# Performance work log

Measured on AMD Instinct MI355X. Metric: run time of the kernel, lower is better.

Reference implementation:

```python
import jax, jax.numpy as jnp
import numpy as np
import math

B, T, C, H = 4, 2048, 768, 12
D = C // H  # 64 head dim

def setup_inputs() -> dict:
    key = jax.random.key(0)
    k1, k2, k3 = jax.random.split(key, 3)
    x = jax.random.normal(k1, (B, T, C), dtype=jnp.float32)
    mask = jnp.tril(jnp.ones((T, T), dtype=bool))[None, None, :, :]  # causal [1,1,T,T]
    W_attn = jax.random.normal(k2, (C, 3 * C), dtype=jnp.float32) * 0.02
    b_attn = jnp.zeros((3 * C,), dtype=jnp.float32)
    W_proj = jax.random.normal(k3, (C, C), dtype=jnp.float32) * (0.02 / math.sqrt(2 * 12))
    b_proj = jnp.zeros((C,), dtype=jnp.float32)
    return {"x": x, "mask": mask, "W_attn": W_attn, "b_attn": b_attn,
            "W_proj": W_proj, "b_proj": b_proj}

def reference(x, mask, W_attn, b_attn, W_proj, b_proj):
    Bx, Tx, Cx = x.shape
    qkv = x @ W_attn + b_attn                       # [B,T,3C]
    qkv = qkv.reshape(Bx, Tx, 3 * H, D).transpose(0, 2, 1, 3)  # [B,3H,T,D]
    q, k, v = jnp.array_split(qkv, 3, axis=1)       # each [B,H,T,D]
    att = jnp.einsum('bhqd,bhkd->bhqk', q, k) / math.sqrt(D)  # [B,H,T,T]
    att = jnp.where(mask == 0, -jnp.inf, att)
    att = jax.nn.softmax(att, axis=-1)
    y = jnp.einsum('bhqk,bhkd->bhqd', att, v)       # [B,H,T,D]
    y = y.transpose(0, 2, 1, 3).reshape(Bx, Tx, Cx)
    return y @ W_proj + b_proj
```

## Files before the change

### kernel.cpp

```cpp
#include <hip/hip_runtime.h>
#include <math.h>

#define BB 4
#define TT 2048
#define CC 768
#define HH 12
#define DD 64
#define RS (3 * CC)

typedef __bf16 bf16x8 __attribute__((ext_vector_type(8)));
typedef float f32x4 __attribute__((ext_vector_type(4)));
typedef unsigned short u16x8 __attribute__((ext_vector_type(8)));

union U8 { bf16x8 v; u16x8 s; unsigned short u[8]; };
union BCV { __bf16 h; unsigned short u; };

__device__ __forceinline__ unsigned short f2bf(float f) {
  union { float f; unsigned u; } x; x.f = f;
  unsigned r = x.u + 0x7fffu + ((x.u >> 16) & 1u);
  return (unsigned short)(r >> 16);
}

#define AS1 __attribute__((address_space(1)))
#define AS3 __attribute__((address_space(3)))
__device__ __forceinline__ void gl_lds16(const void* g, void* l) {
  __builtin_amdgcn_global_load_lds((const AS1 unsigned int*)g,
                                   (AS3 unsigned int*)l, 16, 0, 0);
}

__global__ __launch_bounds__(256) void cvt_bf16_kernel(
    const float* __restrict__ in, unsigned short* __restrict__ out, int n8) {
  int i = blockIdx.x * 256 + threadIdx.x;
  const int stride = gridDim.x * 256;
  for (; i < n8; i += stride) {
    const float4 a = reinterpret_cast<const float4*>(in)[i * 2];
    const float4 b = reinterpret_cast<const float4*>(in)[i * 2 + 1];
    U8 p;
    p.u[0] = f2bf(a.x); p.u[1] = f2bf(a.y); p.u[2] = f2bf(a.z); p.u[3] = f2bf(a.w);
    p.u[4] = f2bf(b.x); p.u[5] = f2bf(b.y); p.u[6] = f2bf(b.z); p.u[7] = f2bf(b.w);
    reinterpret_cast<u16x8*>(out)[i] = p.s;
  }
}

__global__ __launch_bounds__(256) void transpose_cvt_kernel(
    const float* __restrict__ in, unsigned short* __restrict__ out,
    int K, int N) {
  __shared__ float T[64][65];
  const int k0 = blockIdx.y * 64, n0 = blockIdx.x * 64;
  const int tid = threadIdx.x;
  const int ty = tid >> 4, tx4 = (tid & 15) * 4;
#pragma unroll
  for (int i = 0; i < 4; ++i) {
    const int r = ty + i * 16;
    const float4 v = *reinterpret_cast<const float4*>(
        &in[(size_t)(k0 + r) * N + n0 + tx4]);
    T[r][tx4] = v.x; T[r][tx4 + 1] = v.y; T[r][tx4 + 2] = v.z; T[r][tx4 + 3] = v.w;
  }
  __syncthreads();
  const int nrow = tid >> 2, kc = (tid & 3) * 16;
  U8 p0, p1;
#pragma unroll
  for (int i = 0; i < 8; ++i) {
    p0.u[i] = f2bf(T[kc + i][nrow]);
    p1.u[i] = f2bf(T[kc + 8 + i][nrow]);
  }
  unsigned short* o = &out[(size_t)(n0 + nrow) * K + k0 + kc];
  *reinterpret_cast<u16x8*>(o) = p0.s;
  *reinterpret_cast<u16x8*>(o + 8) = p1.s;
}

__global__ __launch_bounds__(256) void vtrans_kernel(
    const unsigned short* __restrict__ qkvb, unsigned short* __restrict__ Vg) {
  __shared__ unsigned short Tt[64][72];
  const int tok0 = blockIdx.x * 64;
  const int bh = blockIdx.y, b = bh / HH, h = bh % HH;
  const int tid = threadIdx.x;
  const int r = tid >> 2, c = (tid & 3) * 16;
  const unsigned short* src =
      qkvb + (size_t)(b * TT + tok0 + r) * RS + (2 * HH + h) * DD + c;
  *reinterpret_cast<u16x8*>(&Tt[r][c]) = *reinterpret_cast<const u16x8*>(src);
  *reinterpret_cast<u16x8*>(&Tt[r][c + 8]) =
      *reinterpret_cast<const u16x8*>(src + 8);
  __syncthreads();
  const int d = tid >> 2, tc = (tid & 3) * 16;
  U8 o0, o1;
#pragma unroll
  for (int i = 0; i < 8; ++i) {
    o0.u[i] = Tt[tc + i][d];
    o1.u[i] = Tt[tc + 8 + i][d];
  }
  unsigned short* dst = Vg + ((size_t)bh * DD + d) * TT + tok0 + tc;
  *reinterpret_cast<u16x8*>(dst) = o0.s;
  *reinterpret_cast<u16x8*>(dst + 8) = o1.s;
}

template <typename OutT>
__global__ __launch_bounds__(256) void gemm_mfma_kernel(
    const unsigned short* __restrict__ A, const unsigned short* __restrict__ Bt,
    const float* __restrict__ bias, OutT* __restrict__ C,
    int M, int N, int K) {
  __shared__ unsigned short As[2][128 * 32];
  __shared__ unsigned short Bs[2][128 * 32];

  const int tid = threadIdx.x;
  const int w = tid >> 6, l = tid & 63, lr = l & 15, lg = l >> 4;
  const int wr = w >> 1, wc = w & 1;
  const int brow = blockIdx.y * 128, bcol = blockIdx.x * 128;

  f32x4 acc[4][4];
#pragma unroll
  for (int i = 0; i < 4; ++i)
#pragma unroll
    for (int j = 0; j < 4; ++j) acc[i][j] = (f32x4)(0.f);

  const int r0 = tid >> 2, c8 = (tid & 3) * 8;
  const unsigned short* gA = A + (size_t)(brow + r0) * K + c8;
  const unsigned short* gB = Bt + (size_t)(bcol + r0) * K + c8;

  gl_lds16(gA, As[0] + w * 512);
  gl_lds16(gA + (size_t)64 * K, As[0] + w * 512 + 2048);
  gl_lds16(gB, Bs[0] + w * 512);
  gl_lds16(gB + (size_t)64 * K, Bs[0] + w * 512 + 2048);
  __syncthreads();

  int cur = 0;
  for (int k0 = 0; k0 < K; k0 += 32) {
    if (k0 + 32 < K) {
      const int kn = k0 + 32;
      gl_lds16(gA + kn, As[cur ^ 1] + w * 512);
      gl_lds16(gA + (size_t)64 * K + kn, As[cur ^ 1] + w * 512 + 2048);
      gl_lds16(gB + kn, Bs[cur ^ 1] + w * 512);
      gl_lds16(gB + (size_t)64 * K + kn, Bs[cur ^ 1] + w * 512 + 2048);
    }

    bf16x8 af[4], bf[4];
#pragma unroll
    for (int mf = 0; mf < 4; ++mf)
      af[mf] = *reinterpret_cast<const bf16x8*>(
          &As[cur][(wr * 64 + mf * 16 + lr) * 32 + lg * 8]);
#pragma unroll
    for (int nf = 0; nf < 4; ++nf)
      bf[nf] = *reinterpret_cast<const bf16x8*>(
          &Bs[cur][(wc * 64 + nf * 16 + lr) * 32 + lg * 8]);
#pragma unroll
    for (int mf = 0; mf < 4; ++mf)
#pragma unroll
      for (int nf = 0; nf < 4; ++nf)
        acc[mf][nf] = __builtin_amdgcn_mfma_f32_16x16x32_bf16(
            af[mf], bf[nf], acc[mf][nf], 0, 0, 0);

    __syncthreads();
    cur ^= 1;
  }

#pragma unroll
  for (int nf = 0; nf < 4; ++nf) {
    const int col = bcol + wc * 64 + nf * 16 + lr;
    const float bv = bias[col];
#pragma unroll
    for (int mf = 0; mf < 4; ++mf) {
      const int row0 = brow + wr * 64 + mf * 16 + lg * 4;
#pragma unroll
      for (int r = 0; r < 4; ++r) {
        const float v = acc[mf][nf][r] + bv;
        if constexpr (sizeof(OutT) == 2)
          C[(size_t)(row0 + r) * N + col] = (OutT)f2bf(v);
        else
          C[(size_t)(row0 + r) * N + col] = (OutT)v;
      }
    }
  }
}

constexpr int KVT = 64;

__global__ __launch_bounds__(256) void attn_mfma_kernel(
    const unsigned short* __restrict__ qkv,
    const unsigned short* __restrict__ Vg,
    unsigned short* __restrict__ y) {
  __shared__ unsigned short Ks[KVT * 64];
  __shared__ unsigned short Vt[DD * 64];
  __shared__ unsigned short Pl[4 * 16 * 64];

  const int tid = threadIdx.x;
  const int w = tid >> 6, l = tid & 63;
  const int lr = l & 15, lg = l >> 4;
  const int bh = blockIdx.x, b = bh / HH, h = bh % HH;
  const int g = 31 - blockIdx.y;
  const int qw = g * 64 + w * 16;

  const unsigned short* qbase = qkv + (size_t)b * TT * RS + h * DD;
  const unsigned short* kbase = qkv + (size_t)b * TT * RS + (HH + h) * DD;
  const unsigned short* vgb = Vg + (size_t)bh * DD * TT;

  const float qscale = 0.125f * 1.44269504f;
  const int e = lg ^ (lr & 7);
  const int e4 = e ^ 4;

  bf16x8 qf[2];
  {
    const unsigned short* qrow = qbase + (size_t)(qw + lr) * RS;
    qf[0] = *reinterpret_cast<const bf16x8*>(qrow + lg * 8);
    qf[1] = *reinterpret_cast<const bf16x8*>(qrow + lg * 8 + 32);
  }

  f32x4 O[4];
  f32x4 ls = (f32x4)(0.f);
#pragma unroll
  for (int nb = 0; nb < 4; ++nb) O[nb] = (f32x4)(0.f);

  const int srow = tid >> 2, sc2 = (tid & 3) * 2;
  const int sw = srow & 7;
  const int sidx0 = srow * 64 + 8 * (sc2 ^ sw);
  const int sidx1 = srow * 64 + 8 * ((sc2 + 1) ^ sw);
  const int scol = (tid & 3) * 16;
  const unsigned short* kptr = kbase + (size_t)srow * RS + scol;
  const unsigned short* vptr = vgb + (size_t)srow * TT + scol;

  const int ntiles = g + 1;
  u16x8 kr0 = *reinterpret_cast<const u16x8*>(kptr);
  u16x8 kr1 = *reinterpret_cast<const u16x8*>(kptr + 8);
  u16x8 vr0 = *reinterpret_cast<const u16x8*>(vptr);
  u16x8 vr1 = *reinterpret_cast<const u16x8*>(vptr + 8);

  for (int t = 0; t < ntiles; ++t) {
    const int kv0 = t * KVT;
    __syncthreads();
    *reinterpret_cast<u16x8*>(&Ks[sidx0]) = kr0;
    *reinterpret_cast<u16x8*>(&Ks[sidx1]) = kr1;
    *reinterpret_cast<u16x8*>(&Vt[sidx0]) = vr0;
    *reinterpret_cast<u16x8*>(&Vt[sidx1]) = vr1;
    if (t + 1 < ntiles) {
      kptr += (size_t)KVT * RS;
      vptr += KVT;
      kr0 = *reinterpret_cast<const u16x8*>(kptr);
      kr1 = *reinterpret_cast<const u16x8*>(kptr + 8);
      vr0 = *reinterpret_cast<const u16x8*>(vptr);
      vr1 = *reinterpret_cast<const u16x8*>(vptr + 8);
    }
    __syncthreads();

    const bool diag = (t == g);
    const int nbmax = diag ? (w + 1) : 4;

    f32x4 s[4];
#pragma unroll
    for (int nb = 0; nb < 4; ++nb) s[nb] = (f32x4)(0.f);
    __builtin_amdgcn_s_setprio(1);
#pragma unroll
    for (int nb = 0; nb < 4; ++nb) {
      if (nb >= nbmax) continue;
      const int krow = (nb * 16 + lr) * 64;
      const bf16x8 k0 = *reinterpret_cast<const bf16x8*>(&Ks[krow + 8 * e]);
      const bf16x8 k1 = *reinterpret_cast<const bf16x8*>(&Ks[krow + 8 * e4]);
      s[nb] = __builtin_amdgcn_mfma_f32_16x16x32_bf16(qf[0], k0, s[nb], 0, 0, 0);
      s[nb] = __builtin_amdgcn_mfma_f32_16x16x32_bf16(qf[1], k1, s[nb], 0, 0, 0);
    }
    __builtin_amdgcn_s_setprio(0);

    if (diag) {
      const int qrow = qw + lg * 4;
#pragma unroll
      for (int nb = 0; nb < 4; ++nb) {
        if (nb >= nbmax) continue;
        const int key = kv0 + nb * 16 + lr;
#pragma unroll
        for (int r = 0; r < 4; ++r)
          if (key > qrow + r) s[nb][r] = -1e30f;
      }
    }
#pragma unroll
    for (int r = 0; r < 4; ++r) {
      const int prow = lg * 4 + r;
      const int pswz = (prow & 7) << 3;
      unsigned short* pbase = &Pl[w * 1024 + prow * 64];
#pragma unroll
      for (int nb = 0; nb < 4; ++nb) {
        if (nb >= nbmax) {
          pbase[(nb * 16 + lr) ^ pswz] = 0;
          continue;
        }
        const float p = exp2f(s[nb][r] * qscale);
        ls[r] += p;
        BCV cv; cv.h = (__bf16)p;
        pbase[(nb * 16 + lr) ^ pswz] = cv.u;
      }
    }

    asm volatile("s_waitcnt lgkmcnt(0)" ::: "memory");

    {
      const unsigned short* pw = &Pl[w * 1024];
      const bf16x8 pa0 = *reinterpret_cast<const bf16x8*>(&pw[lr * 64 + 8 * e]);
      const bf16x8 pa1 = *reinterpret_cast<const bf16x8*>(&pw[lr * 64 + 8 * e4]);
      __builtin_amdgcn_s_setprio(1);
#pragma unroll
      for (int nb = 0; nb < 4; ++nb) {
        const int vrow = (nb * 16 + lr) * 64;
        const bf16x8 v0 = *reinterpret_cast<const bf16x8*>(&Vt[vrow + 8 * e]);
        const bf16x8 v1 = *reinterpret_cast<const bf16x8*>(&Vt[vrow + 8 * e4]);
        O[nb] = __builtin_amdgcn_mfma_f32_16x16x32_bf16(pa0, v0, O[nb], 0, 0, 0);
        O[nb] = __builtin_amdgcn_mfma_f32_16x16x32_bf16(pa1, v1, O[nb], 0, 0, 0);
      }
      __builtin_amdgcn_s_setprio(0);
    }
  }

#pragma unroll
  for (int off = 1; off < 16; off <<= 1)
#pragma unroll
    for (int r = 0; r < 4; ++r) ls[r] += __shfl_xor(ls[r], off, 64);
  f32x4 inv;
#pragma unroll
  for (int r = 0; r < 4; ++r) inv[r] = 1.f / ls[r];
#pragma unroll
  for (int nb = 0; nb < 4; ++nb)
#pragma unroll
    for (int r = 0; r < 4; ++r)
      y[((size_t)b * TT + qw + lg * 4 + r) * CC + h * DD + nb * 16 + lr] =
          f2bf(O[nb][r] * inv[r]);
}

extern "C" void kernel_launch(void* const* d_in, const int* in_sizes, int n_in,
                              void* d_out, int out_size, void* d_ws, size_t ws_size,
                              hipStream_t stream) {
  const float* x      = (const float*)d_in[0];
  const float* W_attn = (const float*)d_in[2];
  const float* b_attn = (const float*)d_in[3];
  const float* W_proj = (const float*)d_in[4];
  const float* b_proj = (const float*)d_in[5];
  float* out = (float*)d_out;

  const int M = BB * TT;
  unsigned short* qkvb = (unsigned short*)d_ws;
  unsigned short* xb   = qkvb + (size_t)M * RS;
  unsigned short* yb   = xb + (size_t)M * CC;
  unsigned short* Wt1  = yb + (size_t)M * CC;
  unsigned short* Wt2  = Wt1 + (size_t)RS * CC;
  unsigned short* Vg   = xb;

  cvt_bf16_kernel<<<1024, 256, 0, stream>>>(x, xb, M * CC / 8);
  transpose_cvt_kernel<<<dim3(RS / 64, CC / 64), 256, 0, stream>>>(
      W_attn, Wt1, CC, RS);
  transpose_cvt_kernel<<<dim3(CC / 64, CC / 64), 256, 0, stream>>>(
      W_proj, Wt2, CC, CC);

  gemm_mfma_kernel<unsigned short><<<dim3(RS / 128, M / 128), 256, 0, stream>>>(
      xb, Wt1, b_attn, qkvb, M, RS, CC);

  vtrans_kernel<<<dim3(TT / 64, BB * HH), 256, 0, stream>>>(qkvb, Vg);

  attn_mfma_kernel<<<dim3(BB * HH, 32), 256, 0, stream>>>(qkvb, Vg, yb);

  gemm_mfma_kernel<float><<<dim3(CC / 128, M / 128), 256, 0, stream>>>(
      yb, Wt2, b_proj, out, M, CC, CC);
}
```

Measured before the change: 151.4 us.

## Fuse V transpose into QKV GEMM epilogue and prescale Q

```diff
diff --git a/kernel.cpp b/kernel.cpp
--- a/kernel.cpp
+++ b/kernel.cpp
@@ -11,6 +11,7 @@
 typedef __bf16 bf16x8 __attribute__((ext_vector_type(8)));
 typedef float f32x4 __attribute__((ext_vector_type(4)));
 typedef unsigned short u16x8 __attribute__((ext_vector_type(8)));
+typedef unsigned short u16x4 __attribute__((ext_vector_type(4)));
 
 union U8 { bf16x8 v; u16x8 s; unsigned short u[8]; };
 union BCV { __bf16 h; unsigned short u; };
@@ -19,6 +20,10 @@
   union { float f; unsigned u; } x; x.f = f;
   unsigned r = x.u + 0x7fffu + ((x.u >> 16) & 1u);
   return (unsigned short)(r >> 16);
+}
+__device__ __forceinline__ float bf2f(unsigned short u) {
+  union { unsigned u; float f; } x; x.u = (unsigned)u << 16;
+  return x.f;
 }
 
 #define AS1 __attribute__((address_space(1)))
@@ -69,36 +74,10 @@
   *reinterpret_cast<u16x8*>(o + 8) = p1.s;
 }
 
-__global__ __launch_bounds__(256) void vtrans_kernel(
-    const unsigned short* __restrict__ qkvb, unsigned short* __restrict__ Vg) {
-  __shared__ unsigned short Tt[64][72];
-  const int tok0 = blockIdx.x * 64;
-  const int bh = blockIdx.y, b = bh / HH, h = bh % HH;
-  const int tid = threadIdx.x;
-  const int r = tid >> 2, c = (tid & 3) * 16;
-  const unsigned short* src =
-      qkvb + (size_t)(b * TT + tok0 + r) * RS + (2 * HH + h) * DD + c;
-  *reinterpret_cast<u16x8*>(&Tt[r][c]) = *reinterpret_cast<const u16x8*>(src);
-  *reinterpret_cast<u16x8*>(&Tt[r][c + 8]) =
-      *reinterpret_cast<const u16x8*>(src + 8);
-  __syncthreads();
-  const int d = tid >> 2, tc = (tid & 3) * 16;
-  U8 o0, o1;
-#pragma unroll
-  for (int i = 0; i < 8; ++i) {
-    o0.u[i] = Tt[tc + i][d];
-    o1.u[i] = Tt[tc + 8 + i][d];
-  }
-  unsigned short* dst = Vg + ((size_t)bh * DD + d) * TT + tok0 + tc;
-  *reinterpret_cast<u16x8*>(dst) = o0.s;
-  *reinterpret_cast<u16x8*>(dst + 8) = o1.s;
-}
-
-template <typename OutT>
-__global__ __launch_bounds__(256) void gemm_mfma_kernel(
+__global__ __launch_bounds__(256) void gemm1_kernel(
     const unsigned short* __restrict__ A, const unsigned short* __restrict__ Bt,
-    const float* __restrict__ bias, OutT* __restrict__ C,
-    int M, int N, int K) {
+    const float* __restrict__ bias, unsigned short* __restrict__ Cq,
+    unsigned short* __restrict__ Vg, int M, int N, int K) {
   __shared__ unsigned short As[2][128 * 32];
   __shared__ unsigned short Bs[2][128 * 32];
 
@@ -153,6 +132,97 @@
     cur ^= 1;
   }
 
+  if (bcol >= 2 * CC) {
+    const int bloc = brow >> 11;
+    const int tokw = (brow & 2047) + wr * 64;
+#pragma unroll
+    for (int nf = 0; nf < 4; ++nf) {
+      const int hd = bcol - 2 * CC + wc * 64 + nf * 16 + lr;
+      const float bv = bias[bcol + wc * 64 + nf * 16 + lr];
+      unsigned short* vdst =
+          Vg + ((size_t)(bloc * HH + (hd >> 6)) * DD + (hd & 63)) * TT + tokw;
+#pragma unroll
+      for (int mf = 0; mf < 4; ++mf) {
+        u16x4 pk;
+#pragma unroll
+        for (int r = 0; r < 4; ++r) pk[r] = f2bf(acc[mf][nf][r] + bv);
+        *reinterpret_cast<u16x4*>(vdst + mf * 16 + lg * 4) = pk;
+      }
+    }
+  } else {
+#pragma unroll
+    for (int nf = 0; nf < 4; ++nf) {
+      const int col = bcol + wc * 64 + nf * 16 + lr;
+      const float bv = bias[col];
+#pragma unroll
+      for (int mf = 0; mf < 4; ++mf) {
+        const int row0 = brow + wr * 64 + mf * 16 + lg * 4;
+#pragma unroll
+        for (int r = 0; r < 4; ++r)
+          Cq[(size_t)(row0 + r) * N + col] = f2bf(acc[mf][nf][r] + bv);
+      }
+    }
+  }
+}
+
+__global__ __launch_bounds__(256) void gemm2_kernel(
+    const unsigned short* __restrict__ A, const unsigned short* __restrict__ Bt,
+    const float* __restrict__ bias, float* __restrict__ C,
+    int M, int N, int K) {
+  __shared__ unsigned short As[2][128 * 32];
+  __shared__ unsigned short Bs[2][128 * 32];
+
+  const int tid = threadIdx.x;
+  const int w = tid >> 6, l = tid & 63, lr = l & 15, lg = l >> 4;
+  const int wr = w >> 1, wc = w & 1;
+  const int brow = blockIdx.y * 128, bcol = blockIdx.x * 128;
+
+  f32x4 acc[4][4];
+#pragma unroll
+  for (int i = 0; i < 4; ++i)
+#pragma unroll
+    for (int j = 0; j < 4; ++j) acc[i][j] = (f32x4)(0.f);
+
+  const int r0 = tid >> 2, c8 = (tid & 3) * 8;
+  const unsigned short* gA = A + (size_t)(brow + r0) * K + c8;
+  const unsigned short* gB = Bt + (size_t)(bcol + r0) * K + c8;
+
+  gl_lds16(gA, As[0] + w * 512);
+  gl_lds16(gA + (size_t)64 * K, As[0] + w * 512 + 2048);
+  gl_lds16(gB, Bs[0] + w * 512);
+  gl_lds16(gB + (size_t)64 * K, Bs[0] + w * 512 + 2048);
+  __syncthreads();
+
+  int cur = 0;
+  for (int k0 = 0; k0 < K; k0 += 32) {
+    if (k0 + 32 < K) {
+      const int kn = k0 + 32;
+      gl_lds16(gA + kn, As[cur ^ 1] + w * 512);
+      gl_lds16(gA + (size_t)64 * K + kn, As[cur ^ 1] + w * 512 + 2048);
+      gl_lds16(gB + kn, Bs[cur ^ 1] + w * 512);
+      gl_lds16(gB + (size_t)64 * K + kn, Bs[cur ^ 1] + w * 512 + 2048);
+    }
+
+    bf16x8 af[4], bf[4];
+#pragma unroll
+    for (int mf = 0; mf < 4; ++mf)
+      af[mf] = *reinterpret_cast<const bf16x8*>(
+          &As[cur][(wr * 64 + mf * 16 + lr) * 32 + lg * 8]);
+#pragma unroll
+    for (int nf = 0; nf < 4; ++nf)
+      bf[nf] = *reinterpret_cast<const bf16x8*>(
+          &Bs[cur][(wc * 64 + nf * 16 + lr) * 32 + lg * 8]);
+#pragma unroll
+    for (int mf = 0; mf < 4; ++mf)
+#pragma unroll
+      for (int nf = 0; nf < 4; ++nf)
+        acc[mf][nf] = __builtin_amdgcn_mfma_f32_16x16x32_bf16(
+            af[mf], bf[nf], acc[mf][nf], 0, 0, 0);
+
+    __syncthreads();
+    cur ^= 1;
+  }
+
 #pragma unroll
   for (int nf = 0; nf < 4; ++nf) {
     const int col = bcol + wc * 64 + nf * 16 + lr;
@@ -161,13 +231,8 @@
     for (int mf = 0; mf < 4; ++mf) {
       const int row0 = brow + wr * 64 + mf * 16 + lg * 4;
 #pragma unroll
-      for (int r = 0; r < 4; ++r) {
-        const float v = acc[mf][nf][r] + bv;
-        if constexpr (sizeof(OutT) == 2)
-          C[(size_t)(row0 + r) * N + col] = (OutT)f2bf(v);
-        else
-          C[(size_t)(row0 + r) * N + col] = (OutT)v;
-      }
+      for (int r = 0; r < 4; ++r)
+        C[(size_t)(row0 + r) * N + col] = acc[mf][nf][r] + bv;
     }
   }
 }
@@ -200,8 +265,14 @@
   bf16x8 qf[2];
   {
     const unsigned short* qrow = qbase + (size_t)(qw + lr) * RS;
-    qf[0] = *reinterpret_cast<const bf16x8*>(qrow + lg * 8);
-    qf[1] = *reinterpret_cast<const bf16x8*>(qrow + lg * 8 + 32);
+#pragma unroll
+    for (int hf = 0; hf < 2; ++hf) {
+      const u16x8 raw = *reinterpret_cast<const u16x8*>(qrow + lg * 8 + hf * 32);
+      U8 t;
+#pragma unroll
+      for (int i = 0; i < 8; ++i) t.u[i] = f2bf(bf2f(raw[i]) * qscale);
+      qf[hf] = t.v;
+    }
   }
 
   f32x4 O[4];
@@ -280,7 +351,7 @@
           pbase[(nb * 16 + lr) ^ pswz] = 0;
           continue;
         }
-        const float p = exp2f(s[nb][r] * qscale);
+        const float p = exp2f(s[nb][r]);
         ls[r] += p;
         BCV cv; cv.h = (__bf16)p;
         pbase[(nb * 16 + lr) ^ pswz] = cv.u;
@@ -337,7 +408,7 @@
   unsigned short* yb   = xb + (size_t)M * CC;
   unsigned short* Wt1  = yb + (size_t)M * CC;
   unsigned short* Wt2  = Wt1 + (size_t)RS * CC;
-  unsigned short* Vg   = xb;
+  unsigned short* Vg   = Wt2 + (size_t)CC * CC;
 
   cvt_bf16_kernel<<<1024, 256, 0, stream>>>(x, xb, M * CC / 8);
   transpose_cvt_kernel<<<dim3(RS / 64, CC / 64), 256, 0, stream>>>(
@@ -345,13 +416,11 @@
   transpose_cvt_kernel<<<dim3(CC / 64, CC / 64), 256, 0, stream>>>(
       W_proj, Wt2, CC, CC);
 
-  gemm_mfma_kernel<unsigned short><<<dim3(RS / 128, M / 128), 256, 0, stream>>>(
-      xb, Wt1, b_attn, qkvb, M, RS, CC);
-
-  vtrans_kernel<<<dim3(TT / 64, BB * HH), 256, 0, stream>>>(qkvb, Vg);
+  gemm1_kernel<<<dim3(RS / 128, M / 128), 256, 0, stream>>>(
+      xb, Wt1, b_attn, qkvb, Vg, M, RS, CC);
 
   attn_mfma_kernel<<<dim3(BB * HH, 32), 256, 0, stream>>>(qkvb, Vg, yb);
 
-  gemm_mfma_kernel<float><<<dim3(CC / 128, M / 128), 256, 0, stream>>>(
+  gemm2_kernel<<<dim3(CC / 128, M / 128), 256, 0, stream>>>(
       yb, Wt2, b_proj, out, M, CC, CC);
 }
```

Measured after the change: 153.0 us. No clear change (+1.1%).
